# Optimization experiments

Measured on AMD Instinct MI355X. Metric: run time of the kernel, lower is better.

The kernel has to match this reference:

```python
import jax, jax.numpy as jnp
import numpy as np

N_EMBED = 1024
HEAD_SIZE = 64


def setup_inputs() -> dict:
    key = jax.random.key(0)
    ks = jax.random.split(key, 7)
    scale = 1.0 / np.sqrt(N_EMBED)
    x = jax.random.normal(ks[0], (4, 4096, N_EMBED), dtype=jnp.float32)
    Wq = jax.random.uniform(ks[1], (N_EMBED, HEAD_SIZE), jnp.float32, -scale, scale)
    bq = jax.random.uniform(ks[2], (HEAD_SIZE,), jnp.float32, -scale, scale)
    Wk = jax.random.uniform(ks[3], (N_EMBED, HEAD_SIZE), jnp.float32, -scale, scale)
    bk = jax.random.uniform(ks[4], (HEAD_SIZE,), jnp.float32, -scale, scale)
    Wv = jax.random.uniform(ks[5], (N_EMBED, HEAD_SIZE), jnp.float32, -scale, scale)
    bv = jax.random.uniform(ks[6], (HEAD_SIZE,), jnp.float32, -scale, scale)
    return {"x": x, "Wq": Wq, "bq": bq, "Wk": Wk, "bk": bk, "Wv": Wv, "bv": bv}


def reference(x, Wq, bq, Wk, bk, Wv, bv):
    B, T, C = x.shape
    q = x @ Wq + bq                      # [B,T,H]
    k = x @ Wk + bk                      # [B,T,H]
    v = x @ Wv + bv                      # [B,T,H]
    inv_sqrt_h = jnp.asarray(k.shape[-1] ** -0.5, dtype=x.dtype)
    scores = jnp.einsum('bqh,bkh->bqk', q, k) * inv_sqrt_h  # [B,T,T]
    causal = jnp.tril(jnp.ones((T, T), dtype=bool))
    scores = jnp.where(causal, scores, jnp.asarray(-jnp.inf, dtype=x.dtype))
    weights = jax.nn.softmax(scores, axis=-1)
    # dropout p=0.0 -> identity
    out = jnp.einsum('bqk,bkh->bqh', weights, v)  # [B,T,H]
    return out
```

## Files before the change

kernel.cpp:

```cpp
#include <hip/hip_runtime.h>
#include <hip/hip_bf16.h>
#include <stdint.h>

#define DI __device__ __forceinline__

typedef __attribute__((ext_vector_type(8))) short short8;
typedef __attribute__((ext_vector_type(4))) short short4v;
typedef __attribute__((ext_vector_type(4))) float f32x4;
typedef __attribute__((ext_vector_type(16))) float f32x16;

static constexpr int TT = 4096;
static constexpr int CC = 1024;
static constexpr int HH = 64;

DI short f2b(float x) {
  __hip_bfloat16 h = __float2bfloat16(x);
  return __builtin_bit_cast(short, h);
}
DI unsigned packbf(float lo, float hi) {
  return (unsigned)(unsigned short)f2b(lo) |
         ((unsigned)(unsigned short)f2b(hi) << 16);
}

DI f32x4 MFMA(short8 a, short8 b, f32x4 c) {
  return __builtin_amdgcn_mfma_f32_16x16x32_bf16(a, b, c, 0, 0, 0);
}
DI f32x16 MFMA32(short8 a, short8 b, f32x16 c) {
  return __builtin_amdgcn_mfma_f32_32x32x16_bf16(a, b, c, 0, 0, 0);
}

__global__ __launch_bounds__(256) void prep_wt(const float* __restrict__ Wq,
                                               const float* __restrict__ Wk,
                                               const float* __restrict__ Wv,
                                               short* __restrict__ Wt) {
  int o = blockIdx.x * 256 + threadIdx.x;
  int mat = o >> 16;
  int rem = o & 65535;
  int n = rem >> 10;
  int k = rem & 1023;
  const float* W = (mat == 0) ? Wq : ((mat == 1) ? Wk : Wv);
  Wt[o] = f2b(W[k * HH + n]);
}

__global__ __launch_bounds__(256, 2) void qkv_gemm(const float* __restrict__ x,
                                                   const short* __restrict__ Wt,
                                                   const float* __restrict__ bq,
                                                   const float* __restrict__ bk,
                                                   const float* __restrict__ bv,
                                                   short* __restrict__ qbuf,
                                                   short* __restrict__ kbuf,
                                                   short* __restrict__ vT) {
  __shared__ float lds_acc[2][32 * 196];

  const int tid = threadIdx.x;
  const int w = tid >> 6, lane = tid & 63;
  const int c = lane & 15, g = lane >> 4;
  const int m0 = blockIdx.x * 32;
  const int kb0 = w * 256;

  f32x4 acc[2][12] = {};

#pragma unroll
  for (int s8 = 0; s8 < 8; ++s8) {
    const int k0 = kb0 + s8 * 32;
    short8 afr[2];
#pragma unroll
    for (int mf = 0; mf < 2; ++mf) {
      const float* ap = x + (size_t)(m0 + 16 * mf + c) * CC + k0 + 8 * g;
      float4 a0 = ((const float4*)ap)[0];
      float4 a1 = ((const float4*)ap)[1];
      short8 p;
      p[0] = f2b(a0.x); p[1] = f2b(a0.y); p[2] = f2b(a0.z); p[3] = f2b(a0.w);
      p[4] = f2b(a1.x); p[5] = f2b(a1.y); p[6] = f2b(a1.z); p[7] = f2b(a1.w);
      afr[mf] = p;
    }
#pragma unroll
    for (int nf = 0; nf < 12; ++nf) {
      const int mat = nf >> 2;
      const int nn = (nf & 3) * 16 + c;
      short8 bfr = *(const short8*)(Wt + mat * 65536 + nn * CC + k0 + 8 * g);
      acc[0][nf] = MFMA(afr[0], bfr, acc[0][nf]);
      acc[1][nf] = MFMA(afr[1], bfr, acc[1][nf]);
    }
  }

  float* bufA = lds_acc[0];
  float* bufB = lds_acc[1];
  if (w >= 2) {
    float* buf = (w == 2) ? bufA : bufB;
#pragma unroll
    for (int mf = 0; mf < 2; ++mf)
#pragma unroll
      for (int nf = 0; nf < 12; ++nf)
#pragma unroll
        for (int r = 0; r < 4; ++r)
          buf[(16 * mf + 4 * g + r) * 196 + 16 * nf + c] = acc[mf][nf][r];
  }
  __syncthreads();
  if (w < 2) {
    float* buf = (w == 0) ? bufA : bufB;
#pragma unroll
    for (int mf = 0; mf < 2; ++mf)
#pragma unroll
      for (int nf = 0; nf < 12; ++nf)
#pragma unroll
        for (int r = 0; r < 4; ++r)
          buf[(16 * mf + 4 * g + r) * 196 + 16 * nf + c] += acc[mf][nf][r];
  }
  __syncthreads();

  const float QSCALE = 0.125f * 1.44269504088896340736f;
  const int bb = m0 >> 12;
  const int t0 = m0 & 4095;
  if (w < 3) {
    const int n = lane;
    const int cg = w * 64 + n;
    const float* bp = (w == 0) ? bq : ((w == 1) ? bk : bv);
    const float bias = bp[n];
    const float scale = (w == 0) ? QSCALE : 1.0f;
    if (w < 2) {
      short* op = (w == 0) ? qbuf : kbuf;
#pragma unroll
      for (int row = 0; row < 32; ++row) {
        float v = bufA[row * 196 + cg] + bufB[row * 196 + cg];
        op[(size_t)(m0 + row) * HH + n] = f2b((v + bias) * scale);
      }
    } else {
#pragma unroll
      for (int r4 = 0; r4 < 8; ++r4) {
        short4v pv;
#pragma unroll
        for (int j = 0; j < 4; ++j) {
          int row = 4 * r4 + j;
          float v = bufA[row * 196 + cg] + bufB[row * 196 + cg];
          pv[j] = f2b(v + bias);
        }
        *(short4v*)(vT + (size_t)(bb * HH + n) * TT + t0 + 4 * r4) = pv;
      }
    }
  }
}

__global__ __launch_bounds__(256, 2) void attn(const short* __restrict__ qbuf,
                                               const short* __restrict__ kbuf,
                                               const short* __restrict__ vT,
                                               float* __restrict__ out) {
  __shared__ short lds_pt[4 * 32 * 40];
  __shared__ float4 lds_od[3 * 8 * 64];
  __shared__ float lds_ml[3 * 128];

  const int id = blockIdx.x;
  const int xcd = id & 7, slot = id >> 3;
  const int rix = (slot < 32) ? slot : (95 - slot);
  const int rank = rix * 8 + xcd;
  const int jj = 127 - (rank >> 2);
  const int bb = rank & 3;

  const int tid = threadIdx.x;
  const int w = tid >> 6, lane = tid & 63;
  const int ql = lane & 31;
  const int hi = lane >> 5;
  const int q0 = jj * 32;
  const int nT = jj + 1;
  const int tlo = (w * nT) >> 2, thi = ((w + 1) * nT) >> 2;

  const short* qr = qbuf + (size_t)(bb * TT + q0 + ql) * HH + 8 * hi;
  const short8 qf0 = *(const short8*)(qr);
  const short8 qf1 = *(const short8*)(qr + 16);
  const short8 qf2 = *(const short8*)(qr + 32);
  const short8 qf3 = *(const short8*)(qr + 48);

  const short* kB = kbuf + (size_t)bb * TT * HH;
  const short* vB = vT + (size_t)bb * HH * TT;

  f32x16 accO0 = {0,0,0,0,0,0,0,0,0,0,0,0,0,0,0,0};
  f32x16 accO1 = {0,0,0,0,0,0,0,0,0,0,0,0,0,0,0,0};
  float m = -INFINITY, l = 0.f;

  short* ptw = lds_pt + w * 1280;

  for (int t = tlo; t < thi; ++t) {
    const int kv0 = t * 32;
    const short* krow = kB + (size_t)(kv0 + ql) * HH + 8 * hi;
    short8 kf0 = *(const short8*)(krow);
    short8 kf1 = *(const short8*)(krow + 16);
    short8 kf2 = *(const short8*)(krow + 32);
    short8 kf3 = *(const short8*)(krow + 48);
    const short* vrow = vB + (size_t)ql * TT + kv0 + 8 * hi;
    short8 vf00 = *(const short8*)(vrow);
    short8 vf01 = *(const short8*)(vrow + 16);
    short8 vf10 = *(const short8*)(vrow + 32 * TT);
    short8 vf11 = *(const short8*)(vrow + 32 * TT + 16);

    f32x16 sc = {0,0,0,0,0,0,0,0,0,0,0,0,0,0,0,0};
    sc = MFMA32(kf0, qf0, sc);
    sc = MFMA32(kf1, qf1, sc);
    sc = MFMA32(kf2, qf2, sc);
    sc = MFMA32(kf3, qf3, sc);

    if (t == nT - 1) {
#pragma unroll
      for (int r = 0; r < 16; ++r) {
        int kt = kv0 + (r & 3) + 8 * (r >> 2) + 4 * hi;
        if (kt > q0 + ql) sc[r] = -INFINITY;
      }
    }

    float tm = fmaxf(fmaxf(fmaxf(sc[0], sc[1]), fmaxf(sc[2], sc[3])),
                     fmaxf(fmaxf(sc[4], sc[5]), fmaxf(sc[6], sc[7])));
    float tm2 = fmaxf(fmaxf(fmaxf(sc[8], sc[9]), fmaxf(sc[10], sc[11])),
                      fmaxf(fmaxf(sc[12], sc[13]), fmaxf(sc[14], sc[15])));
    tm = fmaxf(tm, tm2);
    tm = fmaxf(tm, __shfl_xor(tm, 32));
    if (__any(tm > m + 8.0f)) {
      float mn = fmaxf(m, tm);
      float al = exp2f(m - mn);
      l *= al;
#pragma unroll
      for (int r = 0; r < 16; ++r) { accO0[r] *= al; accO1[r] *= al; }
      m = mn;
    }
    float p[16];
    float rs = 0.f;
#pragma unroll
    for (int r = 0; r < 16; ++r) {
      p[r] = exp2f(sc[r] - m);
      rs += p[r];
    }
    l += rs + __shfl_xor(rs, 32);

#pragma unroll
    for (int rg = 0; rg < 4; ++rg) {
      uint2 d;
      d.x = packbf(p[4 * rg], p[4 * rg + 1]);
      d.y = packbf(p[4 * rg + 2], p[4 * rg + 3]);
      *(uint2*)(ptw + ql * 40 + 8 * rg + 4 * hi) = d;
    }
    short8 pf0 = *(const short8*)(ptw + ql * 40 + 8 * hi);
    short8 pf1 = *(const short8*)(ptw + ql * 40 + 16 + 8 * hi);

    accO0 = MFMA32(vf00, pf0, accO0);
    accO0 = MFMA32(vf01, pf1, accO0);
    accO1 = MFMA32(vf10, pf0, accO1);
    accO1 = MFMA32(vf11, pf1, accO1);
  }

  __syncthreads();
  if (w > 0) {
#pragma unroll
    for (int rq = 0; rq < 4; ++rq) {
      float4 t0, t1;
      t0.x = accO0[4 * rq]; t0.y = accO0[4 * rq + 1];
      t0.z = accO0[4 * rq + 2]; t0.w = accO0[4 * rq + 3];
      t1.x = accO1[4 * rq]; t1.y = accO1[4 * rq + 1];
      t1.z = accO1[4 * rq + 2]; t1.w = accO1[4 * rq + 3];
      lds_od[((w - 1) * 8 + rq) * 64 + lane] = t0;
      lds_od[((w - 1) * 8 + 4 + rq) * 64 + lane] = t1;
    }
    lds_ml[(w - 1) * 128 + lane] = m;
    lds_ml[(w - 1) * 128 + 64 + lane] = l;
  }
  __syncthreads();
  if (w == 0) {
    float m1 = lds_ml[lane],       l1 = lds_ml[64 + lane];
    float m2 = lds_ml[128 + lane], l2 = lds_ml[192 + lane];
    float m3 = lds_ml[256 + lane], l3 = lds_ml[320 + lane];
    float ms = fmaxf(fmaxf(m, m1), fmaxf(m2, m3));
    float c0 = exp2f(m - ms), c1 = exp2f(m1 - ms);
    float c2 = exp2f(m2 - ms), c3 = exp2f(m3 - ms);
    float inv = 1.0f / (c0 * l + c1 * l1 + c2 * l2 + c3 * l3);
    float* orow = out + (size_t)(bb * TT + q0 + ql) * HH;
#pragma unroll
    for (int rq = 0; rq < 8; ++rq) {
      float4 v1 = lds_od[(0 * 8 + rq) * 64 + lane];
      float4 v2 = lds_od[(1 * 8 + rq) * 64 + lane];
      float4 v3 = lds_od[(2 * 8 + rq) * 64 + lane];
      float o0, o1, o2, o3;
      if (rq < 4) {
        o0 = accO0[4 * (rq & 3)];     o1 = accO0[4 * (rq & 3) + 1];
        o2 = accO0[4 * (rq & 3) + 2]; o3 = accO0[4 * (rq & 3) + 3];
      } else {
        o0 = accO1[4 * (rq & 3)];     o1 = accO1[4 * (rq & 3) + 1];
        o2 = accO1[4 * (rq & 3) + 2]; o3 = accO1[4 * (rq & 3) + 3];
      }
      float4 res;
      res.x = (c0 * o0 + c1 * v1.x + c2 * v2.x + c3 * v3.x) * inv;
      res.y = (c0 * o1 + c1 * v1.y + c2 * v2.y + c3 * v3.y) * inv;
      res.z = (c0 * o2 + c1 * v1.z + c2 * v2.z + c3 * v3.z) * inv;
      res.w = (c0 * o3 + c1 * v1.w + c2 * v2.w + c3 * v3.w) * inv;
      const int ht = rq >> 2, r2 = rq & 3;
      *(float4*)(orow + 32 * ht + 8 * r2 + 4 * hi) = res;
    }
  }
}

extern "C" void kernel_launch(void* const* d_in, const int* in_sizes, int n_in,
                              void* d_out, int out_size, void* d_ws, size_t ws_size,
                              hipStream_t stream) {
  const float* x  = (const float*)d_in[0];
  const float* Wq = (const float*)d_in[1];
  const float* bq = (const float*)d_in[2];
  const float* Wk = (const float*)d_in[3];
  const float* bk = (const float*)d_in[4];
  const float* Wv = (const float*)d_in[5];
  const float* bv = (const float*)d_in[6];
  float* out = (float*)d_out;

  char* ws = (char*)d_ws;
  short* Wt = (short*)ws;
  short* qb = (short*)(ws + 393216);
  short* kb = qb + 16384 * 64;
  short* vT = kb + 16384 * 64;

  prep_wt<<<dim3(768), dim3(256), 0, stream>>>(Wq, Wk, Wv, Wt);
  qkv_gemm<<<dim3(512), dim3(256), 0, stream>>>(x, Wt, bq, bk, bv, qb, kb, vT);
  attn<<<dim3(512), dim3(256), 0, stream>>>(qb, kb, vT, out);
}
```

Measured before the change: 166.0 us.

## Restructure QKV GEMM into LDS-staged double-buffered 64-row tiles

The QKV projection kernel changes from split-K across four waves with an LDS reduction to a 64x192 output tile per 512-thread block. A and B tiles are staged through swizzled, double-buffered LDS, with the weight tile loaded by direct global-to-LDS loads and the next x tile prefetched into registers during the MFMAs. This removes redundant per-wave global reads of the weights and the cross-wave reduction. In exchange it adds a barrier per K step and launches only 256 blocks, which lowers the grid parallelism.

```diff
diff --git a/kernel.cpp b/kernel.cpp
--- a/kernel.cpp
+++ b/kernel.cpp
@@ -27,6 +27,12 @@
 }
 DI f32x16 MFMA32(short8 a, short8 b, f32x16 c) {
   return __builtin_amdgcn_mfma_f32_32x32x16_bf16(a, b, c, 0, 0, 0);
+}
+
+DI void gload_lds16(const void* g, void* l) {
+  __builtin_amdgcn_global_load_lds(
+      (__attribute__((address_space(1))) void*)(void*)(uintptr_t)g,
+      (__attribute__((address_space(3))) void*)(void*)(uintptr_t)l, 16, 0, 0);
 }
 
 __global__ __launch_bounds__(256) void prep_wt(const float* __restrict__ Wq,
@@ -42,7 +48,7 @@
   Wt[o] = f2b(W[k * HH + n]);
 }
 
-__global__ __launch_bounds__(256, 2) void qkv_gemm(const float* __restrict__ x,
+__global__ __launch_bounds__(512, 2) void qkv_gemm(const float* __restrict__ x,
                                                    const short* __restrict__ Wt,
                                                    const float* __restrict__ bq,
                                                    const float* __restrict__ bk,
@@ -50,92 +56,121 @@
                                                    short* __restrict__ qbuf,
                                                    short* __restrict__ kbuf,
                                                    short* __restrict__ vT) {
-  __shared__ float lds_acc[2][32 * 196];
+  __shared__ short lds_a[2 * 64 * 64];
+  __shared__ short lds_b[2 * 192 * 64];
 
   const int tid = threadIdx.x;
   const int w = tid >> 6, lane = tid & 63;
+  const int wr = w >> 2, wc = w & 3;
   const int c = lane & 15, g = lane >> 4;
-  const int m0 = blockIdx.x * 32;
-  const int kb0 = w * 256;
-
-  f32x4 acc[2][12] = {};
-
-#pragma unroll
-  for (int s8 = 0; s8 < 8; ++s8) {
-    const int k0 = kb0 + s8 * 32;
-    short8 afr[2];
-#pragma unroll
-    for (int mf = 0; mf < 2; ++mf) {
-      const float* ap = x + (size_t)(m0 + 16 * mf + c) * CC + k0 + 8 * g;
-      float4 a0 = ((const float4*)ap)[0];
-      float4 a1 = ((const float4*)ap)[1];
-      short8 p;
-      p[0] = f2b(a0.x); p[1] = f2b(a0.y); p[2] = f2b(a0.z); p[3] = f2b(a0.w);
-      p[4] = f2b(a1.x); p[5] = f2b(a1.y); p[6] = f2b(a1.z); p[7] = f2b(a1.w);
-      afr[mf] = p;
-    }
-#pragma unroll
-    for (int nf = 0; nf < 12; ++nf) {
-      const int mat = nf >> 2;
-      const int nn = (nf & 3) * 16 + c;
-      short8 bfr = *(const short8*)(Wt + mat * 65536 + nn * CC + k0 + 8 * g);
-      acc[0][nf] = MFMA(afr[0], bfr, acc[0][nf]);
-      acc[1][nf] = MFMA(afr[1], bfr, acc[1][nf]);
-    }
-  }
-
-  float* bufA = lds_acc[0];
-  float* bufB = lds_acc[1];
-  if (w >= 2) {
-    float* buf = (w == 2) ? bufA : bufB;
+  const int m0 = blockIdx.x * 64;
+  const int ar = tid >> 3, as = tid & 7;
+  const int sw = (c & 7) << 4;
+
+  f32x4 acc[2][3] = {};
+
+  {
+    const float* ap = x + (size_t)(m0 + ar) * CC + 8 * as;
+    float4 a0 = ((const float4*)ap)[0];
+    float4 a1 = ((const float4*)ap)[1];
+    uint2 d0, d1;
+    d0.x = packbf(a0.x, a0.y); d0.y = packbf(a0.z, a0.w);
+    d1.x = packbf(a1.x, a1.y); d1.y = packbf(a1.z, a1.w);
+    uint4 pk = {d0.x, d0.y, d1.x, d1.y};
+    *(uint4*)((char*)lds_a + ar * 128 + ((16 * as) ^ ((ar & 7) << 4))) = pk;
+#pragma unroll
+    for (int ch = 0; ch < 3; ++ch) {
+      int n = ch * 64 + w * 8 + (lane >> 3);
+      int q = lane & 7;
+      gload_lds16(Wt + n * CC + 8 * (q ^ (n & 7)),
+                  lds_b + (ch * 512 + w * 64) * 8);
+    }
+  }
+  __syncthreads();
+
+  for (int t = 0; t < 16; ++t) {
+    const int cur = t & 1, nxt = cur ^ 1;
+    const short* Ab = lds_a + cur * 4096;
+    const short* Bb = lds_b + cur * 12288;
+
+    float4 xa0, xa1;
+    if (t + 1 < 16) {
+      const float* ap = x + (size_t)(m0 + ar) * CC + (t + 1) * 64 + 8 * as;
+      xa0 = ((const float4*)ap)[0];
+      xa1 = ((const float4*)ap)[1];
+#pragma unroll
+      for (int ch = 0; ch < 3; ++ch) {
+        int n = ch * 64 + w * 8 + (lane >> 3);
+        int q = lane & 7;
+        gload_lds16(Wt + n * CC + (t + 1) * 64 + 8 * (q ^ (n & 7)),
+                    lds_b + nxt * 12288 + (ch * 512 + w * 64) * 8);
+      }
+    }
+
+    short8 afr[2][2], bfr[3][2];
 #pragma unroll
     for (int mf = 0; mf < 2; ++mf)
 #pragma unroll
-      for (int nf = 0; nf < 12; ++nf)
-#pragma unroll
-        for (int r = 0; r < 4; ++r)
-          buf[(16 * mf + 4 * g + r) * 196 + 16 * nf + c] = acc[mf][nf][r];
-  }
-  __syncthreads();
-  if (w < 2) {
-    float* buf = (w == 0) ? bufA : bufB;
-#pragma unroll
-    for (int mf = 0; mf < 2; ++mf)
-#pragma unroll
-      for (int nf = 0; nf < 12; ++nf)
-#pragma unroll
-        for (int r = 0; r < 4; ++r)
-          buf[(16 * mf + 4 * g + r) * 196 + 16 * nf + c] += acc[mf][nf][r];
-  }
-  __syncthreads();
+      for (int ks = 0; ks < 2; ++ks) {
+        int row = 32 * wr + 16 * mf + c;
+        afr[mf][ks] = *(const short8*)((const char*)Ab + row * 128 +
+                                       ((ks * 64 + g * 16) ^ sw));
+      }
+#pragma unroll
+    for (int nf = 0; nf < 3; ++nf)
+#pragma unroll
+      for (int ks = 0; ks < 2; ++ks) {
+        int n = 48 * wc + 16 * nf + c;
+        bfr[nf][ks] = *(const short8*)((const char*)Bb + n * 128 +
+                                       ((ks * 64 + g * 16) ^ sw));
+      }
+#pragma unroll
+    for (int ks = 0; ks < 2; ++ks)
+#pragma unroll
+      for (int mf = 0; mf < 2; ++mf)
+#pragma unroll
+        for (int nf = 0; nf < 3; ++nf)
+          acc[mf][nf] = MFMA(afr[mf][ks], bfr[nf][ks], acc[mf][nf]);
+
+    if (t + 1 < 16) {
+      uint2 d0, d1;
+      d0.x = packbf(xa0.x, xa0.y); d0.y = packbf(xa0.z, xa0.w);
+      d1.x = packbf(xa1.x, xa1.y); d1.y = packbf(xa1.z, xa1.w);
+      uint4 pk = {d0.x, d0.y, d1.x, d1.y};
+      *(uint4*)((char*)lds_a + nxt * 8192 + ar * 128 +
+                ((16 * as) ^ ((ar & 7) << 4))) = pk;
+    }
+    __syncthreads();
+  }
 
   const float QSCALE = 0.125f * 1.44269504088896340736f;
   const int bb = m0 >> 12;
   const int t0 = m0 & 4095;
-  if (w < 3) {
-    const int n = lane;
-    const int cg = w * 64 + n;
-    const float* bp = (w == 0) ? bq : ((w == 1) ? bk : bv);
+#pragma unroll
+  for (int nf = 0; nf < 3; ++nf) {
+    const int col0 = 48 * wc + 16 * nf;
+    const int mat = col0 >> 6;
+    const int n = (col0 & 63) + c;
+    const float* bp = (mat == 0) ? bq : ((mat == 1) ? bk : bv);
     const float bias = bp[n];
-    const float scale = (w == 0) ? QSCALE : 1.0f;
-    if (w < 2) {
-      short* op = (w == 0) ? qbuf : kbuf;
-#pragma unroll
-      for (int row = 0; row < 32; ++row) {
-        float v = bufA[row * 196 + cg] + bufB[row * 196 + cg];
-        op[(size_t)(m0 + row) * HH + n] = f2b((v + bias) * scale);
-      }
+    if (mat < 2) {
+      short* op = (mat == 0) ? qbuf : kbuf;
+      const float scale = (mat == 0) ? QSCALE : 1.0f;
+#pragma unroll
+      for (int mf = 0; mf < 2; ++mf)
+#pragma unroll
+        for (int r = 0; r < 4; ++r) {
+          int mrow = m0 + 32 * wr + 16 * mf + 4 * g + r;
+          op[(size_t)mrow * HH + n] = f2b((acc[mf][nf][r] + bias) * scale);
+        }
     } else {
 #pragma unroll
-      for (int r4 = 0; r4 < 8; ++r4) {
+      for (int mf = 0; mf < 2; ++mf) {
         short4v pv;
 #pragma unroll
-        for (int j = 0; j < 4; ++j) {
-          int row = 4 * r4 + j;
-          float v = bufA[row * 196 + cg] + bufB[row * 196 + cg];
-          pv[j] = f2b(v + bias);
-        }
-        *(short4v*)(vT + (size_t)(bb * HH + n) * TT + t0 + 4 * r4) = pv;
+        for (int r = 0; r < 4; ++r) pv[r] = f2b(acc[mf][nf][r] + bias);
+        *(short4v*)(vT + (size_t)(bb * HH + n) * TT + t0 + 32 * wr + 16 * mf +
+                    4 * g) = pv;
       }
     }
   }
@@ -313,6 +348,6 @@
   short* vT = kb + 16384 * 64;
 
   prep_wt<<<dim3(768), dim3(256), 0, stream>>>(Wq, Wk, Wv, Wt);
-  qkv_gemm<<<dim3(512), dim3(256), 0, stream>>>(x, Wt, bq, bk, bv, qb, kb, vT);
+  qkv_gemm<<<dim3(256), dim3(512), 0, stream>>>(x, Wt, bq, bk, bv, qb, kb, vT);
   attn<<<dim3(512), dim3(256), 0, stream>>>(qb, kb, vT, out);
 }
```

New measurement: 150.5 us. 9.3% less time.
